# Kernel tuning notes

Hardware: AMD Instinct MI355X
Metric: run time of the kernel (lower is better)

The kernel has to match this reference:

```python
import jax, jax.numpy as jnp
import numpy as np

B, T, H, NH = 2, 2048, 2048, 16
HD = H // NH  # 128


def setup_inputs() -> dict:
    key = jax.random.key(0)
    ks = jax.random.split(key, 7)
    s = 1.0 / np.sqrt(H)
    return {
        "x": jax.random.normal(ks[0], (B, T, H), jnp.float32),
        "cos": jax.random.uniform(ks[1], (1, 1, T, HD), jnp.float32),
        "sin": jax.random.uniform(ks[2], (1, 1, T, HD), jnp.float32),
        "Wq": jax.random.normal(ks[3], (H, H), jnp.float32) * s,
        "Wk": jax.random.normal(ks[4], (H, H), jnp.float32) * s,
        "Wv": jax.random.normal(ks[5], (H, H), jnp.float32) * s,
        "Wo": jax.random.normal(ks[6], (H, H), jnp.float32) * s,
    }


def rotate_half(x):
    d = x.shape[-1] // 2
    return jnp.concatenate([-x[..., d:], x[..., :d]], axis=-1)


def reference(x, cos, sin, Wq, Wk, Wv, Wo):
    b, t, h = x.shape
    # torch Linear: y = x @ W.T; reshape to (B, NH, T, HD)
    def proj(W):
        return jnp.einsum('bth,oh->bto', x, W).reshape(b, t, NH, HD).transpose(0, 2, 1, 3)
    q, k, v = proj(Wq), proj(Wk), proj(Wv)
    q = q * cos + rotate_half(q) * sin
    k = k * cos + rotate_half(k) * sin
    scale = 1.0 / jnp.sqrt(jnp.asarray(HD, x.dtype))
    scores = jnp.einsum('bhqd,bhkd->bhqk', q, k) * scale  # [B,NH,T,T]
    causal = jnp.tril(jnp.ones((t, t), bool))
    scores = jnp.where(causal, scores, jnp.asarray(-jnp.inf, scores.dtype))
    attn = jax.nn.softmax(scores, axis=-1)
    out = jnp.einsum('bhqk,bhkd->bhqd', attn, v)  # [B,NH,T,HD]
    out = out.transpose(0, 2, 1, 3).reshape(b, t, h)
    return jnp.einsum('bth,oh->bto', out, Wo)
```

## Files before the change

kernel.cpp:

```cpp
#include <hip/hip_runtime.h>
#include <hip/hip_bf16.h>

#define B_  2
#define T_  2048
#define H_  2048
#define NH_ 16
#define HD_ 128
#define QKVN 6144

typedef __attribute__((ext_vector_type(8))) short  short8;
typedef __attribute__((ext_vector_type(4))) float  floatx4;

__device__ __forceinline__ unsigned short f2bf(float x) {
    union { float f; unsigned int u; } c; c.f = x;
    unsigned int r = c.u + 0x7FFF + ((c.u >> 16) & 1);
    return (unsigned short)(r >> 16);
}
__device__ __forceinline__ float bf2f(unsigned short u) {
    union { float f; unsigned int i; } c;
    c.i = ((unsigned int)u) << 16;
    return c.f;
}

__device__ __forceinline__ void gload_lds16(const void* g, void* l) {
    __builtin_amdgcn_global_load_lds(
        (__attribute__((address_space(1))) void*)g,
        (__attribute__((address_space(3))) void*)l, 16, 0, 0);
}

__global__ __launch_bounds__(256) void f32_to_bf16(
    const float* __restrict__ src, unsigned short* __restrict__ dst, int n)
{
    const int i = (blockIdx.x * 256 + threadIdx.x) * 4;
    if (i < n) {
        float4 v = *(const float4*)(src + i);
        ushort4 o;
        o.x = f2bf(v.x); o.y = f2bf(v.y); o.z = f2bf(v.z); o.w = f2bf(v.w);
        *(ushort4*)(dst + i) = o;
    }
}

template<int MB>
__device__ __forceinline__ void ld_a4(short8 (&d)[4][2], const unsigned short* src,
                                      int wm, int n16, int quad)
{
    #pragma unroll
    for (int mi = 0; mi < 4; ++mi)
        #pragma unroll
        for (int ks = 0; ks < 2; ++ks)
            d[mi][ks] = *(const short8*)(src + (wm*128 + (MB+mi)*16 + n16) * 64
                                             + (((ks*4 + quad) ^ (n16 & 7)) * 8));
}
template<int NB>
__device__ __forceinline__ void ld_b2(short8 (&d)[2][2], const unsigned short* src,
                                      int wn, int n16, int quad)
{
    #pragma unroll
    for (int ni = 0; ni < 2; ++ni)
        #pragma unroll
        for (int ks = 0; ks < 2; ++ks)
            d[ni][ks] = *(const short8*)(src + (wn*64 + (NB+ni)*16 + n16) * 64
                                             + (((ks*4 + quad) ^ (n16 & 7)) * 8));
}
template<int MB, int NB>
__device__ __forceinline__ void mfma_q(floatx4 (&acc)[8][4],
                                       const short8 (&a)[4][2],
                                       const short8 (&b)[2][2])
{
    #pragma unroll
    for (int ks = 0; ks < 2; ++ks)
        #pragma unroll
        for (int mi = 0; mi < 4; ++mi)
            #pragma unroll
            for (int ni = 0; ni < 2; ++ni)
                acc[MB+mi][NB+ni] = __builtin_amdgcn_mfma_f32_16x16x32_bf16(
                    a[mi][ks], b[ni][ks], acc[MB+mi][NB+ni], 0, 0, 0);
}

#define BAR()  asm volatile("s_barrier" ::: "memory")
#define LGKM0() do { asm volatile("s_waitcnt lgkmcnt(0)" ::: "memory"); \
                     __builtin_amdgcn_sched_barrier(0); } while (0)

template<bool BF16_OUT>
__global__ __launch_bounds__(512, 1) void gemm8(
    const unsigned short* __restrict__ A,
    const unsigned short* __restrict__ W,
    float* __restrict__ Yf, unsigned short* __restrict__ Yb,
    int M, int N, int K)
{
    __shared__ __attribute__((aligned(16))) unsigned short As[2][256 * 64];
    __shared__ __attribute__((aligned(16))) unsigned short Bs[2][256 * 64];

    const int tid  = threadIdx.x;
    const int lane = tid & 63;
    const int n16  = lane & 15;
    const int quad = lane >> 4;
    const int w    = tid >> 6;
    const int wm   = w >> 2;
    const int wn   = w & 3;

    const int m0 = blockIdx.y * 256;
    const int n0 = blockIdx.x * 256;

    const int r0  = tid >> 3;
    const int g0  = ((tid & 7) ^ (r0 & 7)) * 8;
    const unsigned short* A0p = A + (size_t)(m0 + r0) * K + g0;
    const unsigned short* A1p = A + (size_t)(m0 + 64 + r0) * K + g0;
    const unsigned short* B0p = W + (size_t)(n0 + r0) * K + g0;
    const unsigned short* B1p = W + (size_t)(n0 + 64 + r0) * K + g0;
    const size_t hstep = (size_t)128 * K;

    floatx4 acc[8][4];
    #pragma unroll
    for (int i = 0; i < 8; i++)
        #pragma unroll
        for (int j = 0; j < 4; j++) acc[i][j] = (floatx4){0.f, 0.f, 0.f, 0.f};

    const int nt = K >> 6;

    gload_lds16(A0p,         &As[0][(size_t)tid * 8]);
    gload_lds16(A1p,         &As[0][(size_t)(tid + 512) * 8]);
    gload_lds16(A0p + hstep, &As[0][8192 + (size_t)tid * 8]);
    gload_lds16(A1p + hstep, &As[0][8192 + (size_t)(tid + 512) * 8]);
    gload_lds16(B0p,         &Bs[0][(size_t)tid * 8]);
    gload_lds16(B1p,         &Bs[0][(size_t)(tid + 512) * 8]);
    gload_lds16(B0p + hstep, &Bs[0][8192 + (size_t)tid * 8]);
    gload_lds16(B1p + hstep, &Bs[0][8192 + (size_t)(tid + 512) * 8]);
    asm volatile("s_waitcnt vmcnt(0)" ::: "memory");
    BAR();

    for (int t = 0; t < nt; ++t) {
        const unsigned short* Ac = &As[t & 1][0];
        const unsigned short* Bc = &Bs[t & 1][0];
        unsigned short* An = &As[(t & 1) ^ 1][0];
        unsigned short* Bn = &Bs[(t & 1) ^ 1][0];
        const bool pre = (t + 1 < nt);
        const size_t knext = (size_t)(t + 1) << 6;

        short8 afL[4][2], afH[4][2], bfL[2][2], bfH[2][2];

        ld_a4<0>(afL, Ac, wm, n16, quad);
        ld_b2<0>(bfL, Bc, wn, n16, quad);
        if (pre) {
            gload_lds16(A0p + knext,         An + (size_t)tid * 8);
            gload_lds16(A1p + knext,         An + (size_t)(tid + 512) * 8);
            gload_lds16(A0p + knext + hstep, An + 8192 + (size_t)tid * 8);
            gload_lds16(A1p + knext + hstep, An + 8192 + (size_t)(tid + 512) * 8);
        }
        asm volatile("s_waitcnt lgkmcnt(8)" ::: "memory");
        BAR();
        LGKM0();
        __builtin_amdgcn_s_setprio(1);
        mfma_q<0, 0>(acc, afL, bfL);
        __builtin_amdgcn_s_setprio(0);
        BAR();

        ld_b2<2>(bfH, Bc, wn, n16, quad);
        if (pre) {
            gload_lds16(B0p + knext,         Bn + (size_t)tid * 8);
            gload_lds16(B1p + knext,         Bn + (size_t)(tid + 512) * 8);
            gload_lds16(B0p + knext + hstep, Bn + 8192 + (size_t)tid * 8);
            gload_lds16(B1p + knext + hstep, Bn + 8192 + (size_t)(tid + 512) * 8);
        }
        BAR();
        LGKM0();
        __builtin_amdgcn_s_setprio(1);
        mfma_q<0, 2>(acc, afL, bfH);
        __builtin_amdgcn_s_setprio(0);
        BAR();

        ld_a4<4>(afH, Ac, wm, n16, quad);
        BAR();
        LGKM0();
        __builtin_amdgcn_s_setprio(1);
        mfma_q<4, 0>(acc, afH, bfL);
        __builtin_amdgcn_s_setprio(0);
        BAR();

        asm volatile("s_waitcnt vmcnt(0)" ::: "memory");
        BAR();
        __builtin_amdgcn_sched_barrier(0);
        __builtin_amdgcn_s_setprio(1);
        mfma_q<4, 2>(acc, afH, bfH);
        __builtin_amdgcn_s_setprio(0);
        BAR();
    }

    #pragma unroll
    for (int mi = 0; mi < 8; ++mi) {
        const size_t rb = (size_t)(m0 + wm*128 + mi*16 + quad*4);
        #pragma unroll
        for (int r = 0; r < 4; ++r) {
            const size_t row = rb + r;
            #pragma unroll
            for (int ni = 0; ni < 4; ++ni) {
                const size_t col = n0 + wn*64 + ni*16 + n16;
                if (BF16_OUT) Yb[row * N + col] = f2bf(acc[mi][ni][r]);
                else          Yf[row * N + col] = acc[mi][ni][r];
            }
        }
    }
}

__global__ __launch_bounds__(256) void rope_convert_qk(
    const unsigned short* __restrict__ qkvp,
    const float* __restrict__ cosp, const float* __restrict__ sinp,
    unsigned short* __restrict__ qh, unsigned short* __restrict__ kh)
{
    const int idx  = blockIdx.x * 256 + threadIdx.x;
    const int d    = idx & 63;
    const int rest = idx >> 6;
    const int h    = rest & 15;
    const int bt   = rest >> 4;
    const int t    = bt & (T_ - 1);
    const int b    = bt >> 11;
    const size_t ibase = (size_t)bt * QKVN + h * HD_;
    const size_t obase = (((size_t)b * NH_ + h) * T_ + t) * HD_;

    const float c0 = cosp[t*HD_ + d],      s0 = sinp[t*HD_ + d];
    const float c1 = cosp[t*HD_ + d + 64], s1 = sinp[t*HD_ + d + 64];
    const float sc = 0.08838834764831845f;

    float q0 = bf2f(qkvp[ibase + d]), q1 = bf2f(qkvp[ibase + d + 64]);
    qh[obase + d]      = f2bf((q0*c0 - q1*s0) * sc);
    qh[obase + d + 64] = f2bf((q1*c1 + q0*s1) * sc);

    float k0 = bf2f(qkvp[ibase + 2048 + d]), k1 = bf2f(qkvp[ibase + 2048 + d + 64]);
    kh[obase + d]      = f2bf(k0*c0 - k1*s0);
    kh[obase + d + 64] = f2bf(k1*c1 + k0*s1);
}

__global__ __launch_bounds__(256) void transpose_v(
    const unsigned short* __restrict__ qkvp, unsigned short* __restrict__ vh)
{
    __shared__ float tile[64][65];
    const int t0 = blockIdx.x * 64;
    const int d0 = blockIdx.y * 64;
    const int bh = blockIdx.z;
    const int b  = bh >> 4, h = bh & 15;

    for (int i = threadIdx.x; i < 4096; i += 256) {
        int r = i >> 6, c = i & 63;
        tile[r][c] = bf2f(qkvp[((size_t)b*T_ + t0 + r) * QKVN + 4096 + h*HD_ + d0 + c]);
    }
    __syncthreads();
    for (int i = threadIdx.x; i < 4096; i += 256) {
        int dr = i >> 6, tc = i & 63;
        vh[((size_t)bh * HD_ + d0 + dr) * T_ + t0 + tc] = f2bf(tile[tc][dr]);
    }
}

__global__ __launch_bounds__(256, 4) void attn_mfma(
    const unsigned short* __restrict__ qh,
    const unsigned short* __restrict__ kh,
    const unsigned short* __restrict__ vh,
    unsigned short* __restrict__ o)
{
    __shared__ __attribute__((aligned(16))) unsigned short Ks[64 * 128];
    __shared__ __attribute__((aligned(16))) unsigned short Vs[128 * 64];
    __shared__ __attribute__((aligned(16))) unsigned short Ps[4][16 * 64];

    const int tid  = threadIdx.x;
    const int lane = tid & 63;
    const int w    = tid >> 6;
    const int n16  = lane & 15;
    const int quad = lane >> 4;

    const int id   = blockIdx.y * gridDim.x + blockIdx.x;
    const int bh   = id & 31;
    const int a    = (id >> 5) & 7;
    const int u    = id >> 8;
    const int qblk = (u < 2) ? (a + (u << 3)) : ((23 + ((u & 1) << 3)) - a);

    const int q0w  = qblk * 64 + w * 16;

    short8 qf[4];
    {
        const size_t qbase = ((size_t)bh * T_ + q0w + n16) * HD_ + quad * 8;
        #pragma unroll
        for (int c = 0; c < 4; c++)
            qf[c] = *(const short8*)(qh + qbase + c * 32);
    }

    const int rk   = tid >> 4;
    const int gk16 = ((tid & 15) ^ (rk & 7)) * 8;
    const unsigned short* ksrc = kh + (size_t)bh * T_ * HD_ + (size_t)rk * HD_ + gk16;
    const int dv   = tid >> 3;
    const int gv16 = ((tid & 7) ^ (dv & 7)) * 8;
    const unsigned short* vsrc = vh + (size_t)bh * HD_ * T_ + (size_t)dv * T_ + gv16;

    floatx4 of[8];
    #pragma unroll
    for (int i = 0; i < 8; i++) of[i] = (floatx4){0.f, 0.f, 0.f, 0.f};
    float mrow[4], lrow[4];
    #pragma unroll
    for (int r = 0; r < 4; r++) { mrow[r] = -INFINITY; lrow[r] = 0.f; }

    const int nkv = qblk + 1;
    for (int kv = 0; kv < nkv; kv++) {
        const int kv0 = kv * 64;
        __syncthreads();
        #pragma unroll
        for (int it = 0; it < 4; it++)
            gload_lds16(ksrc + (size_t)(kv0 + it * 16) * HD_,
                        Ks + (size_t)(it * 256 + tid) * 8);
        #pragma unroll
        for (int it = 0; it < 4; it++)
            gload_lds16(vsrc + kv0 + (size_t)(it * 32) * T_,
                        Vs + (size_t)(it * 256 + tid) * 8);
        __syncthreads();

        floatx4 s[4];
        #pragma unroll
        for (int kg = 0; kg < 4; kg++) {
            floatx4 acc = {0.f, 0.f, 0.f, 0.f};
            #pragma unroll
            for (int c = 0; c < 4; c++) {
                short8 kf = *(const short8*)(Ks + (kg*16 + n16) * 128
                                                + (((c*4 + quad) ^ (n16 & 7)) * 8));
                acc = __builtin_amdgcn_mfma_f32_16x16x32_bf16(qf[c], kf, acc, 0, 0, 0);
            }
            s[kg] = acc;
        }

        const bool needmask = (kv0 + 63 > q0w);

        float alpha[4];
        #pragma unroll
        for (int r = 0; r < 4; r++) {
            const int qrow = q0w + quad * 4 + r;
            float v0 = s[0][r], v1 = s[1][r], v2 = s[2][r], v3 = s[3][r];
            if (needmask) {
                if (kv0 +  0 + n16 > qrow) v0 = -INFINITY;
                if (kv0 + 16 + n16 > qrow) v1 = -INFINITY;
                if (kv0 + 32 + n16 > qrow) v2 = -INFINITY;
                if (kv0 + 48 + n16 > qrow) v3 = -INFINITY;
            }

            float tm = fmaxf(fmaxf(v0, v1), fmaxf(v2, v3));
            tm = fmaxf(tm, __shfl_xor(tm, 1));
            tm = fmaxf(tm, __shfl_xor(tm, 2));
            tm = fmaxf(tm, __shfl_xor(tm, 4));
            tm = fmaxf(tm, __shfl_xor(tm, 8));

            const float mnew = fmaxf(mrow[r], tm);
            const float aa   = __expf(mrow[r] - mnew);
            const float p0 = __expf(v0 - mnew), p1 = __expf(v1 - mnew);
            const float p2 = __expf(v2 - mnew), p3 = __expf(v3 - mnew);

            float ts = p0 + p1 + p2 + p3;
            ts += __shfl_xor(ts, 1);
            ts += __shfl_xor(ts, 2);
            ts += __shfl_xor(ts, 4);
            ts += __shfl_xor(ts, 8);

            lrow[r] = lrow[r] * aa + ts;
            mrow[r] = mnew;
            alpha[r] = aa;

            const int pr = quad * 4 + r;
            const int sx = pr & 7;
            unsigned short* pp = &Ps[w][pr * 64];
            const int g0p = n16 >> 3, e = n16 & 7;
            pp[((g0p    ) ^ sx) * 8 + e] = f2bf(p0);
            pp[((g0p + 2) ^ sx) * 8 + e] = f2bf(p1);
            pp[((g0p + 4) ^ sx) * 8 + e] = f2bf(p2);
            pp[((g0p + 6) ^ sx) * 8 + e] = f2bf(p3);
        }
        #pragma unroll
        for (int nt = 0; nt < 8; nt++)
            #pragma unroll
            for (int r = 0; r < 4; r++) of[nt][r] *= alpha[r];

        short8 pf0 = *(const short8*)(&Ps[w][n16 * 64 + ((quad       ^ (n16 & 7)) * 8)]);
        short8 pf1 = *(const short8*)(&Ps[w][n16 * 64 + (((quad + 4) ^ (n16 & 7)) * 8)]);
        #pragma unroll
        for (int nt = 0; nt < 8; nt++) {
            const int vr = (nt * 16 + n16) * 64;
            short8 vf0 = *(const short8*)(Vs + vr + ((quad       ^ (n16 & 7)) * 8));
            short8 vf1 = *(const short8*)(Vs + vr + (((quad + 4) ^ (n16 & 7)) * 8));
            of[nt] = __builtin_amdgcn_mfma_f32_16x16x32_bf16(pf0, vf0, of[nt], 0, 0, 0);
            of[nt] = __builtin_amdgcn_mfma_f32_16x16x32_bf16(pf1, vf1, of[nt], 0, 0, 0);
        }
    }

    const int b = bh >> 4, h = bh & 15;
    #pragma unroll
    for (int r = 0; r < 4; r++) {
        const float inv = 1.f / lrow[r];
        const size_t orow = ((size_t)b * T_ + q0w + quad*4 + r) * H_ + h * HD_;
        #pragma unroll
        for (int nt = 0; nt < 8; nt++)
            o[orow + nt*16 + n16] = f2bf(of[nt][r] * inv);
    }
}

extern "C" void kernel_launch(void* const* d_in, const int* in_sizes, int n_in,
                              void* d_out, int out_size, void* d_ws, size_t ws_size,
                              hipStream_t stream)
{
    const float* x    = (const float*)d_in[0];
    const float* cosp = (const float*)d_in[1];
    const float* sinp = (const float*)d_in[2];
    const float* Wq   = (const float*)d_in[3];
    const float* Wk   = (const float*)d_in[4];
    const float* Wv   = (const float*)d_in[5];
    const float* Wo   = (const float*)d_in[6];

    const size_t NEL  = (size_t)B_ * T_ * H_;
    const int    XN   = (int)NEL;
    const int    WN   = H_ * H_;
    char* ws = (char*)d_ws;
    const size_t MB16 = 16777216;

    unsigned short* xh    = (unsigned short*)(ws);
    unsigned short* Wqkvh = (unsigned short*)(ws + MB16);
    unsigned short* Woh   = (unsigned short*)(ws + MB16*5/2);
    unsigned short* qkvp  = (unsigned short*)(ws + 3*MB16);
    unsigned short* kh    = (unsigned short*)(ws + 6*MB16);
    unsigned short* qh    = (unsigned short*)(ws + MB16);
    unsigned short* vh    = (unsigned short*)(ws);
    unsigned short* abh   = (unsigned short*)(ws + 3*MB16);

    f32_to_bf16<<<XN/1024, 256, 0, stream>>>(x,  xh,  XN);
    f32_to_bf16<<<WN/1024, 256, 0, stream>>>(Wq, Wqkvh,          WN);
    f32_to_bf16<<<WN/1024, 256, 0, stream>>>(Wk, Wqkvh +   WN,   WN);
    f32_to_bf16<<<WN/1024, 256, 0, stream>>>(Wv, Wqkvh + 2*WN,   WN);
    f32_to_bf16<<<WN/1024, 256, 0, stream>>>(Wo, Woh,            WN);

    const int M = B_ * T_;

    gemm8<true><<<dim3(QKVN/256, M/256), 512, 0, stream>>>(xh, Wqkvh, nullptr, qkvp, M, QKVN, H_);

    rope_convert_qk<<<(B_*T_*NH_*64)/256, 256, 0, stream>>>(qkvp, cosp, sinp, qh, kh);
    transpose_v<<<dim3(T_/64, HD_/64, B_*NH_), 256, 0, stream>>>(qkvp, vh);

    attn_mfma<<<dim3(T_/64, B_*NH_), 256, 0, stream>>>(qh, kh, vh, abh);

    gemm8<false><<<dim3(H_/256, M/256), 512, 0, stream>>>(abh, Woh, (float*)d_out, nullptr, M, H_, H_);
}
```

Before: 451.1 us.

## Prefetch next tile's low fragments into registers and reorder MFMA quadrants

New measurement: 1.037 ms. +129.8%, slower.

```diff
diff --git a/kernel.cpp b/kernel.cpp
--- a/kernel.cpp
+++ b/kernel.cpp
@@ -77,9 +77,68 @@
                     a[mi][ks], b[ni][ks], acc[MB+mi][NB+ni], 0, 0, 0);
 }
 
-#define BAR()  asm volatile("s_barrier" ::: "memory")
-#define LGKM0() do { asm volatile("s_waitcnt lgkmcnt(0)" ::: "memory"); \
-                     __builtin_amdgcn_sched_barrier(0); } while (0)
+#define BAR()   asm volatile("s_barrier" ::: "memory")
+#define SBAR()  __builtin_amdgcn_sched_barrier(0)
+#define LGKM(n) do { asm volatile("s_waitcnt lgkmcnt(" #n ")" ::: "memory"); SBAR(); } while (0)
+
+__device__ __forceinline__ void g5_tile(
+    const unsigned short* Ac, const unsigned short* Bc,
+    unsigned short* An, unsigned short* Bn,
+    const unsigned short* A0p, const unsigned short* A1p,
+    const unsigned short* B0p, const unsigned short* B1p,
+    size_t hstep, size_t knext, bool pre, int tid,
+    int wm, int wn, int n16, int quad,
+    short8 (&afLc)[4][2], short8 (&bfLc)[2][2],
+    short8 (&afLn)[4][2], short8 (&bfLn)[2][2],
+    short8 (&afH)[4][2],  short8 (&bfH)[2][2],
+    floatx4 (&acc)[8][4])
+{
+    ld_a4<4>(afH, Ac, wm, n16, quad);
+    if (pre) {
+        gload_lds16(A0p + knext,         An + (size_t)tid * 8);
+        gload_lds16(A1p + knext,         An + (size_t)(tid + 512) * 8);
+        gload_lds16(A0p + knext + hstep, An + 8192 + (size_t)tid * 8);
+        gload_lds16(A1p + knext + hstep, An + 8192 + (size_t)(tid + 512) * 8);
+    }
+    BAR();
+    LGKM(8);
+    __builtin_amdgcn_s_setprio(1);
+    mfma_q<0, 0>(acc, afLc, bfLc);
+    __builtin_amdgcn_s_setprio(0);
+    BAR();
+
+    ld_b2<2>(bfH, Bc, wn, n16, quad);
+    if (pre) {
+        gload_lds16(B0p + knext,         Bn + (size_t)tid * 8);
+        gload_lds16(B1p + knext,         Bn + (size_t)(tid + 512) * 8);
+        gload_lds16(B0p + knext + hstep, Bn + 8192 + (size_t)tid * 8);
+        gload_lds16(B1p + knext + hstep, Bn + 8192 + (size_t)(tid + 512) * 8);
+    }
+    BAR();
+    LGKM(4);
+    __builtin_amdgcn_s_setprio(1);
+    mfma_q<4, 0>(acc, afH, bfLc);
+    __builtin_amdgcn_s_setprio(0);
+    BAR();
+
+    LGKM(0);
+    __builtin_amdgcn_s_setprio(1);
+    mfma_q<0, 2>(acc, afLc, bfH);
+    __builtin_amdgcn_s_setprio(0);
+    BAR();
+
+    asm volatile("s_waitcnt vmcnt(0)" ::: "memory");
+    BAR();
+    if (pre) {
+        ld_a4<0>(afLn, An, wm, n16, quad);
+        ld_b2<0>(bfLn, Bn, wn, n16, quad);
+    }
+    SBAR();
+    __builtin_amdgcn_s_setprio(1);
+    mfma_q<4, 2>(acc, afH, bfH);
+    __builtin_amdgcn_s_setprio(0);
+    BAR();
+}
 
 template<bool BF16_OUT>
 __global__ __launch_bounds__(512, 1) void gemm8(
@@ -129,61 +188,21 @@
     asm volatile("s_waitcnt vmcnt(0)" ::: "memory");
     BAR();
 
-    for (int t = 0; t < nt; ++t) {
-        const unsigned short* Ac = &As[t & 1][0];
-        const unsigned short* Bc = &Bs[t & 1][0];
-        unsigned short* An = &As[(t & 1) ^ 1][0];
-        unsigned short* Bn = &Bs[(t & 1) ^ 1][0];
-        const bool pre = (t + 1 < nt);
-        const size_t knext = (size_t)(t + 1) << 6;
-
-        short8 afL[4][2], afH[4][2], bfL[2][2], bfH[2][2];
-
-        ld_a4<0>(afL, Ac, wm, n16, quad);
-        ld_b2<0>(bfL, Bc, wn, n16, quad);
-        if (pre) {
-            gload_lds16(A0p + knext,         An + (size_t)tid * 8);
-            gload_lds16(A1p + knext,         An + (size_t)(tid + 512) * 8);
-            gload_lds16(A0p + knext + hstep, An + 8192 + (size_t)tid * 8);
-            gload_lds16(A1p + knext + hstep, An + 8192 + (size_t)(tid + 512) * 8);
-        }
-        asm volatile("s_waitcnt lgkmcnt(8)" ::: "memory");
-        BAR();
-        LGKM0();
-        __builtin_amdgcn_s_setprio(1);
-        mfma_q<0, 0>(acc, afL, bfL);
-        __builtin_amdgcn_s_setprio(0);
-        BAR();
-
-        ld_b2<2>(bfH, Bc, wn, n16, quad);
-        if (pre) {
-            gload_lds16(B0p + knext,         Bn + (size_t)tid * 8);
-            gload_lds16(B1p + knext,         Bn + (size_t)(tid + 512) * 8);
-            gload_lds16(B0p + knext + hstep, Bn + 8192 + (size_t)tid * 8);
-            gload_lds16(B1p + knext + hstep, Bn + 8192 + (size_t)(tid + 512) * 8);
-        }
-        BAR();
-        LGKM0();
-        __builtin_amdgcn_s_setprio(1);
-        mfma_q<0, 2>(acc, afL, bfH);
-        __builtin_amdgcn_s_setprio(0);
-        BAR();
-
-        ld_a4<4>(afH, Ac, wm, n16, quad);
-        BAR();
-        LGKM0();
-        __builtin_amdgcn_s_setprio(1);
-        mfma_q<4, 0>(acc, afH, bfL);
-        __builtin_amdgcn_s_setprio(0);
-        BAR();
-
-        asm volatile("s_waitcnt vmcnt(0)" ::: "memory");
-        BAR();
-        __builtin_amdgcn_sched_barrier(0);
-        __builtin_amdgcn_s_setprio(1);
-        mfma_q<4, 2>(acc, afH, bfH);
-        __builtin_amdgcn_s_setprio(0);
-        BAR();
+    short8 afL0[4][2], bfL0[2][2], afL1[4][2], bfL1[2][2], afH[4][2], bfH[2][2];
+    ld_a4<0>(afL0, &As[0][0], wm, n16, quad);
+    ld_b2<0>(bfL0, &Bs[0][0], wn, n16, quad);
+
+    for (int t = 0; t < nt; t += 2) {
+        g5_tile(&As[0][0], &Bs[0][0], &As[1][0], &Bs[1][0],
+                A0p, A1p, B0p, B1p, hstep,
+                (size_t)(t + 1) << 6, (t + 1) < nt,
+                tid, wm, wn, n16, quad,
+                afL0, bfL0, afL1, bfL1, afH, bfH, acc);
+        g5_tile(&As[1][0], &Bs[1][0], &As[0][0], &Bs[0][0],
+                A0p, A1p, B0p, B1p, hstep,
+                (size_t)(t + 2) << 6, (t + 2) < nt,
+                tid, wm, wn, n16, quad,
+                afL1, bfL1, afL0, bfL0, afH, bfH, acc);
     }
 
     #pragma unroll
```

## Templatize GEMM tile shape and use smaller tiles for QKV and output projections

Applied to the files above, without the earlier changes.

New measurement: 430.5 us. 4.6% less time.

```diff
diff --git a/kernel.cpp b/kernel.cpp
--- a/kernel.cpp
+++ b/kernel.cpp
@@ -40,56 +40,118 @@
     }
 }
 
-template<int MB>
-__device__ __forceinline__ void ld_a4(short8 (&d)[4][2], const unsigned short* src,
-                                      int wm, int n16, int quad)
-{
-    #pragma unroll
-    for (int mi = 0; mi < 4; ++mi)
+#define BAR()   asm volatile("s_barrier" ::: "memory")
+#define SBAR()  __builtin_amdgcn_sched_barrier(0)
+#define LGKM0() do { asm volatile("s_waitcnt lgkmcnt(0)" ::: "memory"); SBAR(); } while (0)
+#define VM0()   asm volatile("s_waitcnt vmcnt(0)" ::: "memory")
+
+template<int MI, int BASE>
+__device__ __forceinline__ void ldAf(short8 (&d)[MI/2][2], const unsigned short* src,
+                                     int wm, int n16, int quad)
+{
+    #pragma unroll
+    for (int mi = 0; mi < MI/2; ++mi)
         #pragma unroll
         for (int ks = 0; ks < 2; ++ks)
-            d[mi][ks] = *(const short8*)(src + (wm*128 + (MB+mi)*16 + n16) * 64
+            d[mi][ks] = *(const short8*)(src + (wm*(MI*16) + (BASE+mi)*16 + n16) * 64
                                              + (((ks*4 + quad) ^ (n16 & 7)) * 8));
 }
-template<int NB>
-__device__ __forceinline__ void ld_b2(short8 (&d)[2][2], const unsigned short* src,
-                                      int wn, int n16, int quad)
-{
-    #pragma unroll
-    for (int ni = 0; ni < 2; ++ni)
+template<int NI, int BASE>
+__device__ __forceinline__ void ldBf(short8 (&d)[NI/2][2], const unsigned short* src,
+                                     int wn, int n16, int quad)
+{
+    #pragma unroll
+    for (int ni = 0; ni < NI/2; ++ni)
         #pragma unroll
         for (int ks = 0; ks < 2; ++ks)
-            d[ni][ks] = *(const short8*)(src + (wn*64 + (NB+ni)*16 + n16) * 64
+            d[ni][ks] = *(const short8*)(src + (wn*(NI*16) + (BASE+ni)*16 + n16) * 64
                                              + (((ks*4 + quad) ^ (n16 & 7)) * 8));
 }
-template<int MB, int NB>
-__device__ __forceinline__ void mfma_q(floatx4 (&acc)[8][4],
-                                       const short8 (&a)[4][2],
-                                       const short8 (&b)[2][2])
+template<int MI, int NI, int MB, int NB>
+__device__ __forceinline__ void mq(floatx4 (&acc)[MI][NI],
+                                   const short8 (&a)[MI/2][2],
+                                   const short8 (&b)[NI/2][2])
 {
     #pragma unroll
     for (int ks = 0; ks < 2; ++ks)
         #pragma unroll
-        for (int mi = 0; mi < 4; ++mi)
+        for (int mi = 0; mi < MI/2; ++mi)
             #pragma unroll
-            for (int ni = 0; ni < 2; ++ni)
+            for (int ni = 0; ni < NI/2; ++ni)
                 acc[MB+mi][NB+ni] = __builtin_amdgcn_mfma_f32_16x16x32_bf16(
                     a[mi][ks], b[ni][ks], acc[MB+mi][NB+ni], 0, 0, 0);
 }
 
-#define BAR()  asm volatile("s_barrier" ::: "memory")
-#define LGKM0() do { asm volatile("s_waitcnt lgkmcnt(0)" ::: "memory"); \
-                     __builtin_amdgcn_sched_barrier(0); } while (0)
-
-template<bool BF16_OUT>
-__global__ __launch_bounds__(512, 1) void gemm8(
+template<int MI, int NI>
+__device__ __forceinline__ void gt_tile(
+    const unsigned short* Ac, const unsigned short* Bc,
+    unsigned short* An, unsigned short* Bn,
+    const unsigned short* Ap, const unsigned short* Bp,
+    size_t knext, bool pre, int tid, int K,
+    int wm, int wn, int n16, int quad,
+    floatx4 (&acc)[MI][NI])
+{
+    constexpr int MH = MI/2, NH = NI/2;
+    constexpr int AG = (MI*32)/64;
+    constexpr int BG = (NI*64)/64;
+
+    short8 aL[MH][2], aH[MH][2], bL[NH][2], bH[NH][2];
+
+    ldAf<MI, 0>(aL, Ac, wm, n16, quad);
+    ldBf<NI, 0>(bL, Bc, wn, n16, quad);
+    if (pre) {
+        #pragma unroll
+        for (int h = 0; h < AG; ++h)
+            gload_lds16(Ap + knext + (size_t)h * 64 * K, An + h * 4096 + (size_t)tid * 8);
+    }
+    BAR();
+    LGKM0();
+    __builtin_amdgcn_s_setprio(1);
+    mq<MI, NI, 0, 0>(acc, aL, bL);
+    __builtin_amdgcn_s_setprio(0);
+    BAR();
+
+    ldBf<NI, NH>(bH, Bc, wn, n16, quad);
+    if (pre) {
+        #pragma unroll
+        for (int h = 0; h < BG; ++h)
+            gload_lds16(Bp + knext + (size_t)h * 64 * K, Bn + h * 4096 + (size_t)tid * 8);
+    }
+    BAR();
+    LGKM0();
+    __builtin_amdgcn_s_setprio(1);
+    mq<MI, NI, 0, NH>(acc, aL, bH);
+    __builtin_amdgcn_s_setprio(0);
+    BAR();
+
+    ldAf<MI, MH>(aH, Ac, wm, n16, quad);
+    BAR();
+    LGKM0();
+    __builtin_amdgcn_s_setprio(1);
+    mq<MI, NI, MH, 0>(acc, aH, bL);
+    __builtin_amdgcn_s_setprio(0);
+    BAR();
+
+    VM0();
+    BAR();
+    SBAR();
+    __builtin_amdgcn_s_setprio(1);
+    mq<MI, NI, MH, NH>(acc, aH, bH);
+    __builtin_amdgcn_s_setprio(0);
+    BAR();
+}
+
+template<int MI, int NI, bool BF16_OUT>
+__global__ __launch_bounds__(512, 1) void gemm_t(
     const unsigned short* __restrict__ A,
     const unsigned short* __restrict__ W,
     float* __restrict__ Yf, unsigned short* __restrict__ Yb,
     int M, int N, int K)
 {
-    __shared__ __attribute__((aligned(16))) unsigned short As[2][256 * 64];
-    __shared__ __attribute__((aligned(16))) unsigned short Bs[2][256 * 64];
+    constexpr int BM = MI*32, BN = NI*64;
+    constexpr int AG = BM/64, BG = BN/64;
+    __shared__ __attribute__((aligned(16))) unsigned short As[2][BM * 64];
+    __shared__ __attribute__((aligned(16))) unsigned short Bs[2][BN * 64];
 
     const int tid  = threadIdx.x;
     const int lane = tid & 63;
@@ -99,102 +161,49 @@
     const int wm   = w >> 2;
     const int wn   = w & 3;
 
-    const int m0 = blockIdx.y * 256;
-    const int n0 = blockIdx.x * 256;
+    const int m0 = blockIdx.y * BM;
+    const int n0 = blockIdx.x * BN;
 
     const int r0  = tid >> 3;
     const int g0  = ((tid & 7) ^ (r0 & 7)) * 8;
-    const unsigned short* A0p = A + (size_t)(m0 + r0) * K + g0;
-    const unsigned short* A1p = A + (size_t)(m0 + 64 + r0) * K + g0;
-    const unsigned short* B0p = W + (size_t)(n0 + r0) * K + g0;
-    const unsigned short* B1p = W + (size_t)(n0 + 64 + r0) * K + g0;
-    const size_t hstep = (size_t)128 * K;
-
-    floatx4 acc[8][4];
-    #pragma unroll
-    for (int i = 0; i < 8; i++)
-        #pragma unroll
-        for (int j = 0; j < 4; j++) acc[i][j] = (floatx4){0.f, 0.f, 0.f, 0.f};
+    const unsigned short* Ap = A + (size_t)(m0 + r0) * K + g0;
+    const unsigned short* Bp = W + (size_t)(n0 + r0) * K + g0;
+
+    floatx4 acc[MI][NI];
+    #pragma unroll
+    for (int i = 0; i < MI; i++)
+        #pragma unroll
+        for (int j = 0; j < NI; j++) acc[i][j] = (floatx4){0.f, 0.f, 0.f, 0.f};
 
     const int nt = K >> 6;
 
-    gload_lds16(A0p,         &As[0][(size_t)tid * 8]);
-    gload_lds16(A1p,         &As[0][(size_t)(tid + 512) * 8]);
-    gload_lds16(A0p + hstep, &As[0][8192 + (size_t)tid * 8]);
-    gload_lds16(A1p + hstep, &As[0][8192 + (size_t)(tid + 512) * 8]);
-    gload_lds16(B0p,         &Bs[0][(size_t)tid * 8]);
-    gload_lds16(B1p,         &Bs[0][(size_t)(tid + 512) * 8]);
-    gload_lds16(B0p + hstep, &Bs[0][8192 + (size_t)tid * 8]);
-    gload_lds16(B1p + hstep, &Bs[0][8192 + (size_t)(tid + 512) * 8]);
-    asm volatile("s_waitcnt vmcnt(0)" ::: "memory");
-    BAR();
-
-    for (int t = 0; t < nt; ++t) {
-        const unsigned short* Ac = &As[t & 1][0];
-        const unsigned short* Bc = &Bs[t & 1][0];
-        unsigned short* An = &As[(t & 1) ^ 1][0];
-        unsigned short* Bn = &Bs[(t & 1) ^ 1][0];
-        const bool pre = (t + 1 < nt);
-        const size_t knext = (size_t)(t + 1) << 6;
-
-        short8 afL[4][2], afH[4][2], bfL[2][2], bfH[2][2];
-
-        ld_a4<0>(afL, Ac, wm, n16, quad);
-        ld_b2<0>(bfL, Bc, wn, n16, quad);
-        if (pre) {
-            gload_lds16(A0p + knext,         An + (size_t)tid * 8);
-            gload_lds16(A1p + knext,         An + (size_t)(tid + 512) * 8);
-            gload_lds16(A0p + knext + hstep, An + 8192 + (size_t)tid * 8);
-            gload_lds16(A1p + knext + hstep, An + 8192 + (size_t)(tid + 512) * 8);
-        }
-        asm volatile("s_waitcnt lgkmcnt(8)" ::: "memory");
-        BAR();
-        LGKM0();
-        __builtin_amdgcn_s_setprio(1);
-        mfma_q<0, 0>(acc, afL, bfL);
-        __builtin_amdgcn_s_setprio(0);
-        BAR();
-
-        ld_b2<2>(bfH, Bc, wn, n16, quad);
-        if (pre) {
-            gload_lds16(B0p + knext,         Bn + (size_t)tid * 8);
-            gload_lds16(B1p + knext,         Bn + (size_t)(tid + 512) * 8);
-            gload_lds16(B0p + knext + hstep, Bn + 8192 + (size_t)tid * 8);
-            gload_lds16(B1p + knext + hstep, Bn + 8192 + (size_t)(tid + 512) * 8);
-        }
-        BAR();
-        LGKM0();
-        __builtin_amdgcn_s_setprio(1);
-        mfma_q<0, 2>(acc, afL, bfH);
-        __builtin_amdgcn_s_setprio(0);
-        BAR();
-
-        ld_a4<4>(afH, Ac, wm, n16, quad);
-        BAR();
-        LGKM0();
-        __builtin_amdgcn_s_setprio(1);
-        mfma_q<4, 0>(acc, afH, bfL);
-        __builtin_amdgcn_s_setprio(0);
-        BAR();
-
-        asm volatile("s_waitcnt vmcnt(0)" ::: "memory");
-        BAR();
-        __builtin_amdgcn_sched_barrier(0);
-        __builtin_amdgcn_s_setprio(1);
-        mfma_q<4, 2>(acc, afH, bfH);
-        __builtin_amdgcn_s_setprio(0);
-        BAR();
-    }
-
-    #pragma unroll
-    for (int mi = 0; mi < 8; ++mi) {
-        const size_t rb = (size_t)(m0 + wm*128 + mi*16 + quad*4);
+    #pragma unroll
+    for (int h = 0; h < AG; ++h)
+        gload_lds16(Ap + (size_t)h * 64 * K, &As[0][h * 4096 + (size_t)tid * 8]);
+    #pragma unroll
+    for (int h = 0; h < BG; ++h)
+        gload_lds16(Bp + (size_t)h * 64 * K, &Bs[0][h * 4096 + (size_t)tid * 8]);
+    VM0();
+    BAR();
+
+    for (int t = 0; t < nt; t += 2) {
+        gt_tile<MI, NI>(&As[0][0], &Bs[0][0], &As[1][0], &Bs[1][0],
+                        Ap, Bp, (size_t)(t + 1) << 6, (t + 1) < nt,
+                        tid, K, wm, wn, n16, quad, acc);
+        gt_tile<MI, NI>(&As[1][0], &Bs[1][0], &As[0][0], &Bs[0][0],
+                        Ap, Bp, (size_t)(t + 2) << 6, (t + 2) < nt,
+                        tid, K, wm, wn, n16, quad, acc);
+    }
+
+    #pragma unroll
+    for (int mi = 0; mi < MI; ++mi) {
+        const size_t rb = (size_t)(m0 + wm*(MI*16) + mi*16 + quad*4);
         #pragma unroll
         for (int r = 0; r < 4; ++r) {
             const size_t row = rb + r;
             #pragma unroll
-            for (int ni = 0; ni < 4; ++ni) {
-                const size_t col = n0 + wn*64 + ni*16 + n16;
+            for (int ni = 0; ni < NI; ++ni) {
+                const size_t col = n0 + wn*(NI*16) + ni*16 + n16;
                 if (BF16_OUT) Yb[row * N + col] = f2bf(acc[mi][ni][r]);
                 else          Yf[row * N + col] = acc[mi][ni][r];
             }
@@ -430,12 +439,14 @@
 
     const int M = B_ * T_;
 
-    gemm8<true><<<dim3(QKVN/256, M/256), 512, 0, stream>>>(xh, Wqkvh, nullptr, qkvp, M, QKVN, H_);
+    gemm_t<4, 6, true><<<dim3(QKVN/384, M/128), 512, 0, stream>>>(
+        xh, Wqkvh, nullptr, qkvp, M, QKVN, H_);
 
     rope_convert_qk<<<(B_*T_*NH_*64)/256, 256, 0, stream>>>(qkvp, cosp, sinp, qh, kh);
     transpose_v<<<dim3(T_/64, HD_/64, B_*NH_), 256, 0, stream>>>(qkvp, vh);
 
     attn_mfma<<<dim3(T_/64, B_*NH_), 256, 0, stream>>>(qh, kh, vh, abh);
 
-    gemm8<false><<<dim3(H_/256, M/256), 512, 0, stream>>>(abh, Woh, (float*)d_out, nullptr, M, H_, H_);
-}
+    gemm_t<4, 4, false><<<dim3(H_/256, M/128), 512, 0, stream>>>(
+        abh, Woh, (float*)d_out, nullptr, M, H_, H_);
+}
```
